# Kernel optimization log

Measured on AMD Instinct MI355X. Metric: run time of the kernel, lower is better.

Reference implementation:

```python
import jax, jax.numpy as jnp
import numpy as np

SHIFT = 1  # module picks random.random()>0.5 -> +/-1; fixed to +1 for determinism


def setup_inputs() -> dict:
    key = jax.random.key(0)
    k1, k2 = jax.random.split(key)
    x = jax.random.normal(k1, (1, 128, 14, 14), dtype=jnp.float32)
    w = jax.random.normal(k2, (32, 3, 128), dtype=jnp.float32)  # [out_c, kernel, in_c]
    return {"x": x, "w": w}


def reference(x, w):
    # roll + reshape + unfold + permute + einsum chain is equivalent to:
    #   circular roll along W, 1D conv along W (k=3, zero pad 1, 128->32, per H row),
    #   circular roll along H.
    xr = jnp.roll(x, SHIFT, axis=3)
    # w[j,k,i] -> OIHW kernel (32, 128, 1, 3); H kernel size 1, W kernel size 3
    kern = jnp.transpose(w, (0, 2, 1))[:, :, None, :]
    y = jax.lax.conv_general_dilated(
        xr, kern,
        window_strides=(1, 1),
        padding=((0, 0), (1, 1)),
        dimension_numbers=("NCHW", "OIHW", "NCHW"),
    )  # (1, 32, 14, 14)
    return jnp.roll(y, SHIFT, axis=2)
```

## Files before the change

### kernel.cpp

```cpp
#include <hip/hip_runtime.h>


__global__ __launch_bounds__(256) void conv_roll_kernel(
    const float* __restrict__ x,
    const float* __restrict__ wt,
    float* __restrict__ out)
{
    const int t = threadIdx.x;
    const int g = t >> 4;
    const int r = t & 15;

    const int oid = (blockIdx.x << 4) + g;
    const int o   = oid / 196;
    const int rem = oid - o * 196;
    const int h   = rem / 14;
    const int w   = rem - h * 14;

    const int rb = ((h + 13) % 14) * 14;
    const int c0 = rb + ((w + 12) % 14);
    const int c1 = rb + ((w + 13) % 14);
    const int c2 = rb + w;

    const float* __restrict__ wo = wt + o * 384 + r * 8;
    float wv[3][8];
    *reinterpret_cast<float4*>(&wv[0][0]) = *reinterpret_cast<const float4*>(wo);
    *reinterpret_cast<float4*>(&wv[0][4]) = *reinterpret_cast<const float4*>(wo + 4);
    *reinterpret_cast<float4*>(&wv[1][0]) = *reinterpret_cast<const float4*>(wo + 128);
    *reinterpret_cast<float4*>(&wv[1][4]) = *reinterpret_cast<const float4*>(wo + 132);
    *reinterpret_cast<float4*>(&wv[2][0]) = *reinterpret_cast<const float4*>(wo + 256);
    *reinterpret_cast<float4*>(&wv[2][4]) = *reinterpret_cast<const float4*>(wo + 260);

    const float* __restrict__ xb = x + (r * 8) * 196;

    float a0 = 0.f, a1 = 0.f, a2 = 0.f;
#pragma unroll
    for (int j = 0; j < 8; ++j) {
        const float* __restrict__ xp = xb + j * 196;
        a0 = __builtin_fmaf(xp[c0], wv[0][j], a0);
        a1 = __builtin_fmaf(xp[c1], wv[1][j], a1);
        a2 = __builtin_fmaf(xp[c2], wv[2][j], a2);
    }

    float s = a1 + ((w > 0)  ? a0 : 0.f)
                 + ((w < 13) ? a2 : 0.f);

    s += __shfl_xor(s, 1);
    s += __shfl_xor(s, 2);
    s += __shfl_xor(s, 4);
    s += __shfl_xor(s, 8);

    if (r == 0) out[oid] = s;
}

extern "C" void kernel_launch(void* const* d_in, const int* in_sizes, int n_in,
                              void* d_out, int out_size, void* d_ws, size_t ws_size,
                              hipStream_t stream) {
    const float* x  = (const float*)d_in[0];
    const float* wt = (const float*)d_in[1];
    float* out = (float*)d_out;

    conv_roll_kernel<<<392, 256, 0, stream>>>(x, wt, out);
}
```

Measured before the change: 60.22 us.

## Remap threads to output row with shared-memory cross-wave channel reduction

Each block now computes one output row (one out-channel, one H row): a thread handles one W position and one group of 8 input channels. The input reads across lanes become contiguous along W, so loads coalesce better, and the channel reduction moves from xor shuffles plus a shared-memory step across 4 waves. The grid grows from 392 to 448 blocks, and 2 of every 16 lanes do wasted padding work. The change also adds a __syncthreads per block.

```diff
diff --git a/kernel.cpp b/kernel.cpp
--- a/kernel.cpp
+++ b/kernel.cpp
@@ -6,22 +6,23 @@
     const float* __restrict__ wt,
     float* __restrict__ out)
 {
-    const int t = threadIdx.x;
-    const int g = t >> 4;
-    const int r = t & 15;
+    __shared__ float red[64];
 
-    const int oid = (blockIdx.x << 4) + g;
-    const int o   = oid / 196;
-    const int rem = oid - o * 196;
-    const int h   = rem / 14;
-    const int w   = rem - h * 14;
+    const int bx = blockIdx.x;
+    const int o  = bx / 14;
+    const int h  = bx - o * 14;
+    const int rb = ((h + 13) % 14) * 14;
 
-    const int rb = ((h + 13) % 14) * 14;
-    const int c0 = rb + ((w + 12) % 14);
-    const int c1 = rb + ((w + 13) % 14);
-    const int c2 = rb + w;
+    const int t  = threadIdx.x;
+    const int ci = t >> 4;
+    const int w  = t & 15;
 
-    const float* __restrict__ wo = wt + o * 384 + r * 8;
+    const int wc = (w < 14) ? w : 0;
+    const int c0 = rb + ((wc + 12) % 14);
+    const int c1 = rb + ((wc + 13) % 14);
+    const int c2 = rb + wc;
+
+    const float* __restrict__ wo = wt + o * 384 + ci * 8;
     float wv[3][8];
     *reinterpret_cast<float4*>(&wv[0][0]) = *reinterpret_cast<const float4*>(wo);
     *reinterpret_cast<float4*>(&wv[0][4]) = *reinterpret_cast<const float4*>(wo + 4);
@@ -30,7 +31,7 @@
     *reinterpret_cast<float4*>(&wv[2][0]) = *reinterpret_cast<const float4*>(wo + 256);
     *reinterpret_cast<float4*>(&wv[2][4]) = *reinterpret_cast<const float4*>(wo + 260);
 
-    const float* __restrict__ xb = x + (r * 8) * 196;
+    const float* __restrict__ xb = x + (ci * 8) * 196;
 
     float a0 = 0.f, a1 = 0.f, a2 = 0.f;
 #pragma unroll
@@ -43,13 +44,21 @@
 
     float s = a1 + ((w > 0)  ? a0 : 0.f)
                  + ((w < 13) ? a2 : 0.f);
+    if (w >= 14) s = 0.f;
 
-    s += __shfl_xor(s, 1);
-    s += __shfl_xor(s, 2);
-    s += __shfl_xor(s, 4);
-    s += __shfl_xor(s, 8);
+    s += __shfl_down(s, 32);
+    s += __shfl_down(s, 16);
 
-    if (r == 0) out[oid] = s;
+    const int lane = t & 63;
+    const int wave = t >> 6;
+    if (lane < 16) red[wave * 16 + lane] = s;
+
+    __syncthreads();
+
+    if (t < 14) {
+        const float r = red[t] + red[16 + t] + red[32 + t] + red[48 + t];
+        out[o * 196 + h * 14 + t] = r;
+    }
 }
 
 extern "C" void kernel_launch(void* const* d_in, const int* in_sizes, int n_in,
@@ -59,5 +68,5 @@
     const float* wt = (const float*)d_in[1];
     float* out = (float*)d_out;
 
-    conv_roll_kernel<<<392, 256, 0, stream>>>(x, wt, out);
+    conv_roll_kernel<<<448, 256, 0, stream>>>(x, wt, out);
 }
```

New measurement: 56.08 us. -6.9%, faster.
